# Kernel tuning notes

Hardware: AMD Instinct MI355X
Metric: run time of the kernel (lower is better)

The kernel has to match this reference:

```python
import jax, jax.numpy as jnp
import numpy as np

N = 100000   # nodes
E = 1600000  # edges (avg degree 16)
D = 128      # in = hidden = out channels
N_MID = 4    # middle GCN layers (layer_num=6 -> 1 in + 4 mid + 1 out)
BN_EPS = 1e-5


def setup_inputs() -> dict:
    key = jax.random.key(0)
    ks = jax.random.split(key, 6)
    scale = 1.0 / np.sqrt(D)
    x = jax.random.normal(ks[0], (N, D), dtype=jnp.float32)
    edge_index = jax.random.randint(ks[1], (2, E), 0, N, dtype=jnp.int64)
    W0 = jax.random.normal(ks[2], (D, D), dtype=jnp.float32) * scale
    Wmid = jax.random.normal(ks[3], (N_MID, D, D), dtype=jnp.float32) * scale
    Wlast = jax.random.normal(ks[4], (D, D), dtype=jnp.float32) * scale
    return {
        "x": x,
        "edge_index": edge_index,
        "W0": W0,
        "b0": jnp.zeros((D,), jnp.float32),
        "Wmid": Wmid,
        "bmid": jnp.zeros((N_MID, D), jnp.float32),
        "Wlast": Wlast,
        "blast": jnp.zeros((D,), jnp.float32),
        "gamma": jnp.ones((N_MID + 1, D), jnp.float32),
        "beta": jnp.zeros((N_MID + 1, D), jnp.float32),
    }


def _gcn_layer(x, W, b, src, dst, norm, n):
    # GCNConv: h = x @ W; out[dst] += norm_e * h[src]; + bias
    h = x @ W                         # [N, D_out]
    msg = h[src] * norm[:, None]      # [E+N, D_out] gathered + scaled
    return jax.ops.segment_sum(msg, dst, num_segments=n) + b


def _batchnorm(h, g, b):
    # training-mode BatchNorm1d over nodes (biased variance)
    mu = h.mean(axis=0)
    var = h.var(axis=0)
    return (h - mu) * jax.lax.rsqrt(var + BN_EPS) * g + b


def reference(x, edge_index, W0, b0, Wmid, bmid, Wlast, blast, gamma, beta):
    n = x.shape[0]
    # add self-loops (PyG GCNConv default), symmetric normalization
    loop = jnp.arange(n, dtype=edge_index.dtype)
    src = jnp.concatenate([edge_index[0], loop])
    dst = jnp.concatenate([edge_index[1], loop])
    deg = jax.ops.segment_sum(jnp.ones_like(src, dtype=x.dtype), dst, num_segments=n)
    dinv = jnp.where(deg > 0, deg ** -0.5, 0.0)
    norm = dinv[src] * dinv[dst]      # [E+N]

    # layer 0: no residual; dropout is identity in eval (deterministic reference)
    h = _gcn_layer(x, W0, b0, src, dst, norm, n)
    x = jax.nn.relu(_batchnorm(h, gamma[0], beta[0]))
    # middle layers: residual
    for i in range(N_MID):
        h = _gcn_layer(x, Wmid[i], bmid[i], src, dst, norm, n)
        x = jax.nn.relu(_batchnorm(h, gamma[i + 1], beta[i + 1])) + x
    # output layer: no norm/relu
    return _gcn_layer(x, Wlast, blast, src, dst, norm, n)
```

## Files before the change

### kernel.cpp

```cpp
#include <hip/hip_runtime.h>

#define D 128
#define BN_EPS 1e-5f

typedef _Float16 half8 __attribute__((ext_vector_type(8)));
typedef float f32x4 __attribute__((ext_vector_type(4)));
typedef unsigned short ushort_t;
typedef unsigned long long ull_t;

__device__ __forceinline__ unsigned short f2h(float f) {
  union { _Float16 h; unsigned short u; } c;
  c.h = (_Float16)f;
  return c.u;
}
__device__ __forceinline__ unsigned int packh(float lo, float hi) {
  return (unsigned int)f2h(lo) | ((unsigned int)f2h(hi) << 16);
}
__device__ __forceinline__ float h2f(unsigned int v) {
  union { unsigned short u; _Float16 h; } c;
  c.u = (unsigned short)v;
  return (float)c.h;
}

__global__ void k_detect(const int* __restrict__ ei, int* __restrict__ flag) {
  if (blockIdx.x == 0 && threadIdx.x == 0) {
    int is64 = 1;
    for (int i = 0; i < 16; i++)
      if (ei[2 * i + 1] != 0) is64 = 0;
    *flag = is64;
  }
}
__device__ __forceinline__ int load_src(const int* ei, int e, int i, int is64) {
  return is64 ? ei[2 * i] : ei[i];
}
__device__ __forceinline__ int load_dst(const int* ei, int e, int i, int is64) {
  return is64 ? ei[2 * e + 2 * i] : ei[e + i];
}

__global__ void k_hist(const int* __restrict__ ei, int* __restrict__ cnt,
                       const int* __restrict__ flag, int e) {
  int i = blockIdx.x * blockDim.x + threadIdx.x;
  if (i < e) {
    int d = load_dst(ei, e, i, *flag);
    atomicAdd(&cnt[d], 1);
  }
}

__global__ void k_dinv(const int* __restrict__ cnt, float* __restrict__ dinv, int n) {
  int i = blockIdx.x * blockDim.x + threadIdx.x;
  if (i < n) dinv[i] = rsqrtf((float)(cnt[i] + 1));
}

__global__ void k_ordA(const int* __restrict__ cnt, int* __restrict__ dfill,
                       int* __restrict__ bbase, int n, int nb) {
  __shared__ int h[256];
  int t = threadIdx.x;
  h[t] = 0;
  __syncthreads();
  int i = blockIdx.x * 256 + t;
  if (i < n) {
    int d = cnt[i];
    if (d > 255) d = 255;
    atomicAdd(&h[d], 1);
  }
  __syncthreads();
  int c = h[t];
  if (c) bbase[t * nb + blockIdx.x] = atomicAdd(&dfill[t], c);
}

__global__ void k_degscan(const int* __restrict__ dfill, int* __restrict__ dbase) {
  if (blockIdx.x == 0 && threadIdx.x == 0) {
    int run = 0;
    for (int i = 0; i < 256; i++) {
      int t = dfill[i];
      dbase[i] = run;
      run += t;
    }
  }
}

__global__ void k_ordB(const int* __restrict__ cnt, const int* __restrict__ dbase,
                       const int* __restrict__ bbase, unsigned int* __restrict__ ord,
                       int* __restrict__ rank, int* __restrict__ sdeg, int n,
                       int nb) {
  __shared__ int h[256];
  int t = threadIdx.x;
  h[t] = 0;
  __syncthreads();
  int i = blockIdx.x * 256 + t;
  if (i < n) {
    int dc = cnt[i];
    int d = dc > 255 ? 255 : dc;
    int loc = atomicAdd(&h[d], 1);
    int pos = dbase[d] + bbase[d * nb + blockIdx.x] + loc;
    ord[pos] = (unsigned int)i;
    rank[i] = pos;
    sdeg[pos] = dc + 1;
  }
}

__global__ void k_gscan(const int* __restrict__ sdeg, int* __restrict__ gbase,
                        int ngroups, int n) {
  __shared__ int s[256];
  int t = threadIdx.x;
  int per = (ngroups + 255) / 256;
  int g0 = t * per, g1 = g0 + per;
  if (g1 > ngroups) g1 = ngroups;
  int sum = 0;
  for (int g = g0; g < g1; g++) {
    int m = 0;
    for (int j = 0; j < 16; j++) {
      int idx = g * 16 + j;
      int v = (idx < n) ? sdeg[idx] : 0;
      m = max(m, v);
    }
    int st = (m + 1) & ~1;
    gbase[g] = st;
    sum += st * 16;
  }
  s[t] = sum;
  __syncthreads();
  for (int off = 1; off < 256; off <<= 1) {
    int x = (t >= off) ? s[t - off] : 0;
    __syncthreads();
    s[t] += x;
    __syncthreads();
  }
  int run = s[t] - sum;
  for (int g = g0; g < g1; g++) {
    int st = gbase[g];
    gbase[g] = run;
    run += st * 16;
  }
  if (t == 255) gbase[ngroups] = run;
}

__global__ void k_scatter(const int* __restrict__ ei, const int* __restrict__ rank,
                          const int* __restrict__ gbase, int* __restrict__ fill,
                          const float* __restrict__ dinv,
                          unsigned int* __restrict__ eh,
                          const int* __restrict__ flag, int e) {
  int i = blockIdx.x * blockDim.x + threadIdx.x;
  if (i < e) {
    int is64 = *flag;
    int s = load_src(ei, e, i, is64);
    int d = load_dst(ei, e, i, is64);
    int slot = atomicAdd(&fill[d], 1);
    int r = rank[d];
    int g = r >> 4, j = r & 15;
    unsigned int m = ((unsigned int)rank[s] << 15) |
                     (unsigned int)(f2h(dinv[s] * dinv[d]) & 0x7fff);
    __builtin_nontemporal_store(m, &eh[gbase[g] + slot * 16 + j]);
  }
}

__global__ void k_self(const int* __restrict__ cnt, const int* __restrict__ rank,
                       const int* __restrict__ gbase, const float* __restrict__ dinv,
                       unsigned int* __restrict__ eh, int n, int ntot) {
  int i = blockIdx.x * blockDim.x + threadIdx.x;
  if (i >= ntot) return;
  if (i < n) {
    float di = dinv[i];
    int r = rank[i];
    int g = r >> 4, j = r & 15;
    int gb = gbase[g];
    int stride = (gbase[g + 1] - gb) >> 4;
    unsigned int m = ((unsigned int)r << 15) |
                     (unsigned int)(f2h(di * di) & 0x7fff);
    int c = cnt[i];
    __builtin_nontemporal_store(m, &eh[gb + c * 16 + j]);
    for (int s = c + 1; s < stride; s++)
      __builtin_nontemporal_store(0u, &eh[gb + s * 16 + j]);
  } else {
    int g = i >> 4, j = i & 15;
    int gb = gbase[g];
    int stride = (gbase[g + 1] - gb) >> 4;
    for (int s = 0; s < stride; s++)
      __builtin_nontemporal_store(0u, &eh[gb + s * 16 + j]);
  }
}

__global__ void k_wconv(const float* __restrict__ W0, const float* __restrict__ Wmid,
                        const float* __restrict__ Wlast, ushort_t* __restrict__ Wf) {
  int i = blockIdx.x * 256 + threadIdx.x;
  if (i >= 6 * 16384) return;
  int l = i >> 14, r = i & 16383;
  int k = r >> 7, c = r & 127;
  const float* W = (l == 0) ? W0 : (l <= 4 ? Wmid + (size_t)(l - 1) * 16384 : Wlast);
  Wf[(size_t)l * 16384 + (((k >> 3) * 128 + c) << 3) + (k & 7)] = f2h(W[r]);
}

__global__ __launch_bounds__(256) void k_gemm(
    const void* __restrict__ src, const ushort_t* __restrict__ Wf,
    ushort_t* __restrict__ Hh, unsigned int* __restrict__ XhNew,
    const unsigned int* __restrict__ XhPrev, const float* __restrict__ stats,
    const float* __restrict__ gamma, const float* __restrict__ beta,
    const unsigned int* __restrict__ ord, int n, int mode) {
  __shared__ ushort_t As[16384];
  __shared__ ushort_t Ws[16384];
  const int t = threadIdx.x;
  const int rowBase = blockIdx.x * 128;
  const int off = t & 15;
  const size_t slice_stride = (size_t)n * 32;

  float sc[8], sh[8];
  if (mode >= 1) {
    float inv_n = 1.0f / (float)n;
#pragma unroll
    for (int j = 0; j < 8; j++) {
      int ch = off * 8 + j;
      float mean = stats[ch] * inv_n;
      float var = stats[128 + ch] * inv_n - mean * mean;
      if (var < 0.f) var = 0.f;
      float is = rsqrtf(var + BN_EPS);
      float s = gamma[ch] * is;
      sc[j] = s;
      sh[j] = beta[ch] - mean * s;
    }
  }

#pragma unroll
  for (int i = 0; i < 8; i++) {
    int c = t + i * 256;
    int row = c >> 4;
    int grow = rowBase + row;
    bool valid = grow < n;
    if (!valid) grow = n - 1;
    unsigned int pk[4];
    if (mode == 0) {
      int orig = (int)ord[grow];
      const float* xp = (const float*)src + (size_t)orig * 128 + off * 8;
      float4 v0 = *(const float4*)xp;
      float4 v1 = *(const float4*)(xp + 4);
      pk[0] = packh(v0.x, v0.y);
      pk[1] = packh(v0.z, v0.w);
      pk[2] = packh(v1.x, v1.y);
      pk[3] = packh(v1.z, v1.w);
    } else {
      const char* ap = (const char*)src + (size_t)(off >> 1) * slice_stride +
                       (size_t)grow * 32 + (off & 1) * 16;
      uint4 av = *(const uint4*)ap;
      float v[8];
      v[0] = h2f(av.x & 0xffff); v[1] = h2f(av.x >> 16);
      v[2] = h2f(av.y & 0xffff); v[3] = h2f(av.y >> 16);
      v[4] = h2f(av.z & 0xffff); v[5] = h2f(av.z >> 16);
      v[6] = h2f(av.w & 0xffff); v[7] = h2f(av.w >> 16);
#pragma unroll
      for (int j = 0; j < 8; j++) v[j] = fmaxf(v[j] * sc[j] + sh[j], 0.f);
      if (mode == 2) {
        uint4 rv = *(const uint4*)(XhPrev + (size_t)grow * 64 + off * 4);
        v[0] += h2f(rv.x & 0xffff); v[1] += h2f(rv.x >> 16);
        v[2] += h2f(rv.y & 0xffff); v[3] += h2f(rv.y >> 16);
        v[4] += h2f(rv.z & 0xffff); v[5] += h2f(rv.z >> 16);
        v[6] += h2f(rv.w & 0xffff); v[7] += h2f(rv.w >> 16);
      }
      pk[0] = packh(v[0], v[1]);
      pk[1] = packh(v[2], v[3]);
      pk[2] = packh(v[4], v[5]);
      pk[3] = packh(v[6], v[7]);
      if (valid) *(uint4*)(XhNew + (size_t)grow * 64 + off * 4) = *(uint4*)pk;
    }
    *(uint4*)(&As[(off * 128 + row) * 8]) = *(uint4*)pk;
  }
#pragma unroll
  for (int i = 0; i < 8; i++) {
    int c = t + i * 256;
    *(uint4*)(&Ws[c * 8]) = *(const uint4*)(Wf + c * 8);
  }
  __syncthreads();

  const int wave = t >> 6, lane = t & 63;
  const int q = lane >> 4, ln = lane & 15;
  const int m0 = wave * 32;

  f32x4 acc[2][8];
#pragma unroll
  for (int mt = 0; mt < 2; mt++)
#pragma unroll
    for (int nt = 0; nt < 8; nt++) acc[mt][nt] = (f32x4){0.f, 0.f, 0.f, 0.f};

#pragma unroll
  for (int kk = 0; kk < 4; kk++) {
    int kg = kk * 4 + q;
    half8 a[2];
#pragma unroll
    for (int mt = 0; mt < 2; mt++)
      a[mt] = *(const half8*)(&As[(kg * 128 + m0 + mt * 16 + ln) * 8]);
    half8 b[8];
#pragma unroll
    for (int nt = 0; nt < 8; nt++)
      b[nt] = *(const half8*)(&Ws[(kg * 128 + nt * 16 + ln) * 8]);
#pragma unroll
    for (int mt = 0; mt < 2; mt++)
#pragma unroll
      for (int nt = 0; nt < 8; nt++)
        acc[mt][nt] =
            __builtin_amdgcn_mfma_f32_16x16x32_f16(a[mt], b[nt], acc[mt][nt], 0, 0, 0);
  }

#pragma unroll
  for (int mt = 0; mt < 2; mt++) {
#pragma unroll
    for (int r = 0; r < 4; r++) {
      int grow = rowBase + m0 + mt * 16 + q * 4 + r;
      if (grow < n) {
#pragma unroll
        for (int nt = 0; nt < 8; nt++) {
          ushort_t* hp = (ushort_t*)((char*)Hh + (size_t)nt * slice_stride +
                                     (size_t)grow * 32);
          hp[ln] = f2h(acc[mt][nt][r]);
        }
      }
    }
  }
}

__global__ __launch_bounds__(256) void k_agg(const char* __restrict__ hb,
                                             const int* __restrict__ gbase,
                                             const unsigned int* __restrict__ eh,
                                             const unsigned int* __restrict__ ord,
                                             const float* __restrict__ bias,
                                             void* __restrict__ out,
                                             float* __restrict__ stats, int n,
                                             int ngroups, int last) {
  __shared__ float lsum[16], lsq[16];
  const int t = threadIdx.x;
  const int slice = blockIdx.x & 7;
  if (!last) {
    if (t < 16) {
      lsum[t] = 0.f;
      lsq[t] = 0.f;
    }
    __syncthreads();
  }
  const int wave = t >> 6, lane = t & 63;
  const int j = lane >> 2;
  const int c = lane & 3;
  const unsigned int c8 = (unsigned int)c * 8u;
  const size_t plane = (size_t)slice * (size_t)n * 32;
  const char* hbs = hb + plane;
  float4 bv = *(const float4*)(bias + slice * 16 + c * 4);
  float rs0 = 0.f, rs1 = 0.f, rs2 = 0.f, rs3 = 0.f;
  float rq0 = 0.f, rq1 = 0.f, rq2 = 0.f, rq3 = 0.f;

  union HU { uint2 u; _Float16 h[4]; };

  const int nstreams = (gridDim.x >> 3) * 4;
  const int sid = (blockIdx.x >> 3) * 4 + wave;

  for (int gi = sid; gi < ngroups; gi += nstreams) {
    int gb = gbase[gi];
    int dm = (gbase[gi + 1] - gb) >> 4;
    const unsigned int* mp = eh + gb + j;
    float a0 = 0.f, a1 = 0.f, a2 = 0.f, a3 = 0.f;
    int i = 0;
    for (; i + 4 <= dm; i += 4) {
      unsigned int m0 = mp[(i + 0) * 16];
      unsigned int m1 = mp[(i + 1) * 16];
      unsigned int m2 = mp[(i + 2) * 16];
      unsigned int m3 = mp[(i + 3) * 16];
      HU g0, g1, g2, g3;
      g0.u = *(const uint2*)(hbs + (((m0 >> 10) & ~31u) + c8));
      g1.u = *(const uint2*)(hbs + (((m1 >> 10) & ~31u) + c8));
      g2.u = *(const uint2*)(hbs + (((m2 >> 10) & ~31u) + c8));
      g3.u = *(const uint2*)(hbs + (((m3 >> 10) & ~31u) + c8));
      float w0 = h2f(m0 & 0x7fffu);
      float w1 = h2f(m1 & 0x7fffu);
      float w2 = h2f(m2 & 0x7fffu);
      float w3 = h2f(m3 & 0x7fffu);
      a0 = fmaf((float)g0.h[0], w0, a0);
      a1 = fmaf((float)g0.h[1], w0, a1);
      a2 = fmaf((float)g0.h[2], w0, a2);
      a3 = fmaf((float)g0.h[3], w0, a3);
      a0 = fmaf((float)g1.h[0], w1, a0);
      a1 = fmaf((float)g1.h[1], w1, a1);
      a2 = fmaf((float)g1.h[2], w1, a2);
      a3 = fmaf((float)g1.h[3], w1, a3);
      a0 = fmaf((float)g2.h[0], w2, a0);
      a1 = fmaf((float)g2.h[1], w2, a1);
      a2 = fmaf((float)g2.h[2], w2, a2);
      a3 = fmaf((float)g2.h[3], w2, a3);
      a0 = fmaf((float)g3.h[0], w3, a0);
      a1 = fmaf((float)g3.h[1], w3, a1);
      a2 = fmaf((float)g3.h[2], w3, a2);
      a3 = fmaf((float)g3.h[3], w3, a3);
    }
    if (i < dm) {
      unsigned int m0 = mp[(i + 0) * 16];
      unsigned int m1 = mp[(i + 1) * 16];
      HU g0, g1;
      g0.u = *(const uint2*)(hbs + (((m0 >> 10) & ~31u) + c8));
      g1.u = *(const uint2*)(hbs + (((m1 >> 10) & ~31u) + c8));
      float w0 = h2f(m0 & 0x7fffu);
      float w1 = h2f(m1 & 0x7fffu);
      a0 = fmaf((float)g0.h[0], w0, a0);
      a1 = fmaf((float)g0.h[1], w0, a1);
      a2 = fmaf((float)g0.h[2], w0, a2);
      a3 = fmaf((float)g0.h[3], w0, a3);
      a0 = fmaf((float)g1.h[0], w1, a0);
      a1 = fmaf((float)g1.h[1], w1, a1);
      a2 = fmaf((float)g1.h[2], w1, a2);
      a3 = fmaf((float)g1.h[3], w1, a3);
    }
    int oi = gi * 16 + j;
    if (oi < n) {
      a0 += bv.x;
      a1 += bv.y;
      a2 += bv.z;
      a3 += bv.w;
      if (last) {
        int nd = (int)ord[oi];
        float4 ov = {a0, a1, a2, a3};
        *(float4*)((float*)out + (size_t)nd * 128 + slice * 16 + c * 4) = ov;
      } else {
        uint2 ov;
        ov.x = packh(a0, a1);
        ov.y = packh(a2, a3);
        char* op = (char*)out + plane + (size_t)oi * 32 + c8;
        __builtin_nontemporal_store(((unsigned long long)ov.y << 32) | ov.x,
                                    (unsigned long long*)op);
        rs0 += a0; rs1 += a1; rs2 += a2; rs3 += a3;
        rq0 += a0 * a0; rq1 += a1 * a1; rq2 += a2 * a2; rq3 += a3 * a3;
      }
    }
  }

  if (!last) {
    rs0 += __shfl_xor(rs0, 4);  rs1 += __shfl_xor(rs1, 4);
    rs2 += __shfl_xor(rs2, 4);  rs3 += __shfl_xor(rs3, 4);
    rq0 += __shfl_xor(rq0, 4);  rq1 += __shfl_xor(rq1, 4);
    rq2 += __shfl_xor(rq2, 4);  rq3 += __shfl_xor(rq3, 4);
    rs0 += __shfl_xor(rs0, 8);  rs1 += __shfl_xor(rs1, 8);
    rs2 += __shfl_xor(rs2, 8);  rs3 += __shfl_xor(rs3, 8);
    rq0 += __shfl_xor(rq0, 8);  rq1 += __shfl_xor(rq1, 8);
    rq2 += __shfl_xor(rq2, 8);  rq3 += __shfl_xor(rq3, 8);
    rs0 += __shfl_xor(rs0, 16); rs1 += __shfl_xor(rs1, 16);
    rs2 += __shfl_xor(rs2, 16); rs3 += __shfl_xor(rs3, 16);
    rq0 += __shfl_xor(rq0, 16); rq1 += __shfl_xor(rq1, 16);
    rq2 += __shfl_xor(rq2, 16); rq3 += __shfl_xor(rq3, 16);
    rs0 += __shfl_xor(rs0, 32); rs1 += __shfl_xor(rs1, 32);
    rs2 += __shfl_xor(rs2, 32); rs3 += __shfl_xor(rs3, 32);
    rq0 += __shfl_xor(rq0, 32); rq1 += __shfl_xor(rq1, 32);
    rq2 += __shfl_xor(rq2, 32); rq3 += __shfl_xor(rq3, 32);
    if (lane < 4) {
      atomicAdd(&lsum[c * 4 + 0], rs0);
      atomicAdd(&lsum[c * 4 + 1], rs1);
      atomicAdd(&lsum[c * 4 + 2], rs2);
      atomicAdd(&lsum[c * 4 + 3], rs3);
      atomicAdd(&lsq[c * 4 + 0], rq0);
      atomicAdd(&lsq[c * 4 + 1], rq1);
      atomicAdd(&lsq[c * 4 + 2], rq2);
      atomicAdd(&lsq[c * 4 + 3], rq3);
    }
    __syncthreads();
    if (t < 16) {
      atomicAdd(&stats[slice * 16 + t], lsum[t]);
      atomicAdd(&stats[128 + slice * 16 + t], lsq[t]);
    }
  }
}

extern "C" void kernel_launch(void* const* d_in, const int* in_sizes, int n_in,
                              void* d_out, int out_size, void* d_ws, size_t ws_size,
                              hipStream_t stream) {
  const float* x_in = (const float*)d_in[0];
  const int* ei = (const int*)d_in[1];
  const float* W0 = (const float*)d_in[2];
  const float* b0 = (const float*)d_in[3];
  const float* Wmid = (const float*)d_in[4];
  const float* bmid = (const float*)d_in[5];
  const float* Wlast = (const float*)d_in[6];
  const float* blast = (const float*)d_in[7];
  const float* gamma = (const float*)d_in[8];
  const float* beta = (const float*)d_in[9];

  const int n = in_sizes[0] / D;
  const int e = in_sizes[1] / 2;
  const int ngroups = (n + 15) / 16;
  const int ntot = ngroups * 16;
  const int nb = (n + 255) / 256;
  const int ec = e + 10 * n;

  char* ws = (char*)d_ws;
  size_t off = 0;
  auto alloc = [&](size_t bytes) -> void* {
    void* p = ws + off;
    off += (bytes + 255) & ~(size_t)255;
    return p;
  };
  unsigned int* XhA = (unsigned int*)alloc((size_t)n * 64 * 4);
  unsigned int* XhB = (unsigned int*)alloc((size_t)n * 64 * 4);
  unsigned int* Hh = (unsigned int*)alloc((size_t)n * 64 * 4);
  unsigned int* Ag = (unsigned int*)alloc((size_t)n * 64 * 4);
  ushort_t* Wf = (ushort_t*)alloc((size_t)6 * 16384 * 2);
  float* dinv = (float*)alloc((size_t)n * 4);
  int* flag = (int*)alloc(256);
  unsigned int* ord = (unsigned int*)alloc((size_t)ntot * 4);
  int* rank = (int*)alloc((size_t)n * 4);
  int* gbase = (int*)alloc((size_t)(ngroups + 1) * 4);
  int* dbase = (int*)alloc(256 * 4);
  int* bbase = (int*)alloc((size_t)256 * nb * 4);
  unsigned int* eh = (unsigned int*)alloc((size_t)ec * 4);
  int* sdeg = (int*)alloc((size_t)ntot * 4);
  char* zbase = ws + off;
  int* cnt = (int*)alloc((size_t)n * 4);
  int* fill = (int*)alloc((size_t)n * 4);
  int* dfill = (int*)alloc(256 * 4);
  float* stats = (float*)alloc(5 * 256 * 4);
  size_t zbytes = (size_t)((ws + off) - zbase);
  hipMemsetAsync(zbase, 0, zbytes, stream);

  k_detect<<<1, 64, 0, stream>>>(ei, flag);
  int eb = (e + 255) / 256;
  k_hist<<<eb, 256, 0, stream>>>(ei, cnt, flag, e);
  k_dinv<<<nb, 256, 0, stream>>>(cnt, dinv, n);
  k_ordA<<<nb, 256, 0, stream>>>(cnt, dfill, bbase, n, nb);
  k_degscan<<<1, 64, 0, stream>>>(dfill, dbase);
  k_ordB<<<nb, 256, 0, stream>>>(cnt, dbase, bbase, ord, rank, sdeg, n, nb);
  k_gscan<<<1, 256, 0, stream>>>(sdeg, gbase, ngroups, n);
  k_scatter<<<eb, 256, 0, stream>>>(ei, rank, gbase, fill, dinv, eh, flag, e);
  k_self<<<(ntot + 255) / 256, 256, 0, stream>>>(cnt, rank, gbase, dinv, eh, n,
                                                 ntot);
  k_wconv<<<(6 * 16384 + 255) / 256, 256, 0, stream>>>(W0, Wmid, Wlast, Wf);

  const int gemm_blocks = (n + 127) / 128;
  const int agg_blocks = 2048;

  k_gemm<<<gemm_blocks, 256, 0, stream>>>(x_in, Wf, (ushort_t*)Hh, nullptr,
                                          nullptr, nullptr, nullptr, nullptr,
                                          ord, n, 0);
  k_agg<<<agg_blocks, 256, 0, stream>>>((const char*)Hh, gbase, eh, ord, b0, Ag,
                                        stats, n, ngroups, 0);
  unsigned int* xprev = nullptr;
  unsigned int* xnew = XhA;
  for (int L = 1; L <= 4; L++) {
    const float* bL = bmid + (size_t)(L - 1) * D;
    k_gemm<<<gemm_blocks, 256, 0, stream>>>(
        Ag, Wf + (size_t)L * 16384, (ushort_t*)Hh, xnew, xprev,
        stats + (L - 1) * 256, gamma + (L - 1) * D, beta + (L - 1) * D, ord, n,
        (L == 1) ? 1 : 2);
    k_agg<<<agg_blocks, 256, 0, stream>>>((const char*)Hh, gbase, eh, ord, bL,
                                          Ag, stats + L * 256, n, ngroups, 0);
    xprev = xnew;
    xnew = (xnew == XhA) ? XhB : XhA;
  }
  k_gemm<<<gemm_blocks, 256, 0, stream>>>(Ag, Wf + (size_t)5 * 16384,
                                          (ushort_t*)Hh, xnew, xprev,
                                          stats + 4 * 256, gamma + 4 * D,
                                          beta + 4 * D, ord, n, 2);
  k_agg<<<agg_blocks, 256, 0, stream>>>((const char*)Hh, gbase, eh, ord, blast,
                                        d_out, nullptr, n, ngroups, 1);
}
```

Before: 958.3 us.

## Zero edge buffer via memset, plain stores, and unroll aggregation by eight

The padded edge-slot buffer now sits inside the memset-zeroed workspace region, so k_self no longer loops writing zeros into padding slots and only writes the self-loop entry. Scatter and self-loop writes switch from nontemporal to ordinary stores. The aggregation inner loop is unrolled to eight edges per iteration, with a four-step and a two-step tail, so more gathers are in flight. In exchange the memset grows by the full edge buffer size, and the wider unroll raises register pressure in k_agg.

```diff
diff --git a/kernel.cpp b/kernel.cpp
--- a/kernel.cpp
+++ b/kernel.cpp
@@ -150,33 +150,21 @@
     int g = r >> 4, j = r & 15;
     unsigned int m = ((unsigned int)rank[s] << 15) |
                      (unsigned int)(f2h(dinv[s] * dinv[d]) & 0x7fff);
-    __builtin_nontemporal_store(m, &eh[gbase[g] + slot * 16 + j]);
+    eh[gbase[g] + slot * 16 + j] = m;
   }
 }
 
 __global__ void k_self(const int* __restrict__ cnt, const int* __restrict__ rank,
                        const int* __restrict__ gbase, const float* __restrict__ dinv,
-                       unsigned int* __restrict__ eh, int n, int ntot) {
+                       unsigned int* __restrict__ eh, int n) {
   int i = blockIdx.x * blockDim.x + threadIdx.x;
-  if (i >= ntot) return;
   if (i < n) {
     float di = dinv[i];
     int r = rank[i];
     int g = r >> 4, j = r & 15;
-    int gb = gbase[g];
-    int stride = (gbase[g + 1] - gb) >> 4;
     unsigned int m = ((unsigned int)r << 15) |
                      (unsigned int)(f2h(di * di) & 0x7fff);
-    int c = cnt[i];
-    __builtin_nontemporal_store(m, &eh[gb + c * 16 + j]);
-    for (int s = c + 1; s < stride; s++)
-      __builtin_nontemporal_store(0u, &eh[gb + s * 16 + j]);
-  } else {
-    int g = i >> 4, j = i & 15;
-    int gb = gbase[g];
-    int stride = (gbase[g + 1] - gb) >> 4;
-    for (int s = 0; s < stride; s++)
-      __builtin_nontemporal_store(0u, &eh[gb + s * 16 + j]);
+    eh[gbase[g] + cnt[i] * 16 + j] = m;
   }
 }
 
@@ -315,6 +303,18 @@
   }
 }
 
+#define STEP(K)                                                   \
+  {                                                               \
+    unsigned int m_ = mp[(i + K) * 16];                           \
+    HU g_;                                                        \
+    g_.u = *(const uint2*)(hbs + (((m_ >> 10) & ~31u) + c8));     \
+    float w_ = h2f(m_ & 0x7fffu);                                 \
+    a0 = fmaf((float)g_.h[0], w_, a0);                            \
+    a1 = fmaf((float)g_.h[1], w_, a1);                            \
+    a2 = fmaf((float)g_.h[2], w_, a2);                            \
+    a3 = fmaf((float)g_.h[3], w_, a3);                            \
+  }
+
 __global__ __launch_bounds__(256) void k_agg(const char* __restrict__ hb,
                                              const int* __restrict__ gbase,
                                              const unsigned int* __restrict__ eh,
@@ -354,53 +354,51 @@
     const unsigned int* mp = eh + gb + j;
     float a0 = 0.f, a1 = 0.f, a2 = 0.f, a3 = 0.f;
     int i = 0;
-    for (; i + 4 <= dm; i += 4) {
+    for (; i + 8 <= dm; i += 8) {
       unsigned int m0 = mp[(i + 0) * 16];
       unsigned int m1 = mp[(i + 1) * 16];
       unsigned int m2 = mp[(i + 2) * 16];
       unsigned int m3 = mp[(i + 3) * 16];
-      HU g0, g1, g2, g3;
+      unsigned int m4 = mp[(i + 4) * 16];
+      unsigned int m5 = mp[(i + 5) * 16];
+      unsigned int m6 = mp[(i + 6) * 16];
+      unsigned int m7 = mp[(i + 7) * 16];
+      HU g0, g1, g2, g3, g4, g5, g6, g7;
       g0.u = *(const uint2*)(hbs + (((m0 >> 10) & ~31u) + c8));
       g1.u = *(const uint2*)(hbs + (((m1 >> 10) & ~31u) + c8));
       g2.u = *(const uint2*)(hbs + (((m2 >> 10) & ~31u) + c8));
       g3.u = *(const uint2*)(hbs + (((m3 >> 10) & ~31u) + c8));
-      float w0 = h2f(m0 & 0x7fffu);
-      float w1 = h2f(m1 & 0x7fffu);
-      float w2 = h2f(m2 & 0x7fffu);
-      float w3 = h2f(m3 & 0x7fffu);
-      a0 = fmaf((float)g0.h[0], w0, a0);
-      a1 = fmaf((float)g0.h[1], w0, a1);
-      a2 = fmaf((float)g0.h[2], w0, a2);
-      a3 = fmaf((float)g0.h[3], w0, a3);
-      a0 = fmaf((float)g1.h[0], w1, a0);
-      a1 = fmaf((float)g1.h[1], w1, a1);
-      a2 = fmaf((float)g1.h[2], w1, a2);
-      a3 = fmaf((float)g1.h[3], w1, a3);
-      a0 = fmaf((float)g2.h[0], w2, a0);
-      a1 = fmaf((float)g2.h[1], w2, a1);
-      a2 = fmaf((float)g2.h[2], w2, a2);
-      a3 = fmaf((float)g2.h[3], w2, a3);
-      a0 = fmaf((float)g3.h[0], w3, a0);
-      a1 = fmaf((float)g3.h[1], w3, a1);
-      a2 = fmaf((float)g3.h[2], w3, a2);
-      a3 = fmaf((float)g3.h[3], w3, a3);
+      g4.u = *(const uint2*)(hbs + (((m4 >> 10) & ~31u) + c8));
+      g5.u = *(const uint2*)(hbs + (((m5 >> 10) & ~31u) + c8));
+      g6.u = *(const uint2*)(hbs + (((m6 >> 10) & ~31u) + c8));
+      g7.u = *(const uint2*)(hbs + (((m7 >> 10) & ~31u) + c8));
+      float w0 = h2f(m0 & 0x7fffu), w1 = h2f(m1 & 0x7fffu);
+      float w2 = h2f(m2 & 0x7fffu), w3 = h2f(m3 & 0x7fffu);
+      float w4 = h2f(m4 & 0x7fffu), w5 = h2f(m5 & 0x7fffu);
+      float w6 = h2f(m6 & 0x7fffu), w7 = h2f(m7 & 0x7fffu);
+      a0 = fmaf((float)g0.h[0], w0, a0); a1 = fmaf((float)g0.h[1], w0, a1);
+      a2 = fmaf((float)g0.h[2], w0, a2); a3 = fmaf((float)g0.h[3], w0, a3);
+      a0 = fmaf((float)g1.h[0], w1, a0); a1 = fmaf((float)g1.h[1], w1, a1);
+      a2 = fmaf((float)g1.h[2], w1, a2); a3 = fmaf((float)g1.h[3], w1, a3);
+      a0 = fmaf((float)g2.h[0], w2, a0); a1 = fmaf((float)g2.h[1], w2, a1);
+      a2 = fmaf((float)g2.h[2], w2, a2); a3 = fmaf((float)g2.h[3], w2, a3);
+      a0 = fmaf((float)g3.h[0], w3, a0); a1 = fmaf((float)g3.h[1], w3, a1);
+      a2 = fmaf((float)g3.h[2], w3, a2); a3 = fmaf((float)g3.h[3], w3, a3);
+      a0 = fmaf((float)g4.h[0], w4, a0); a1 = fmaf((float)g4.h[1], w4, a1);
+      a2 = fmaf((float)g4.h[2], w4, a2); a3 = fmaf((float)g4.h[3], w4, a3);
+      a0 = fmaf((float)g5.h[0], w5, a0); a1 = fmaf((float)g5.h[1], w5, a1);
+      a2 = fmaf((float)g5.h[2], w5, a2); a3 = fmaf((float)g5.h[3], w5, a3);
+      a0 = fmaf((float)g6.h[0], w6, a0); a1 = fmaf((float)g6.h[1], w6, a1);
+      a2 = fmaf((float)g6.h[2], w6, a2); a3 = fmaf((float)g6.h[3], w6, a3);
+      a0 = fmaf((float)g7.h[0], w7, a0); a1 = fmaf((float)g7.h[1], w7, a1);
+      a2 = fmaf((float)g7.h[2], w7, a2); a3 = fmaf((float)g7.h[3], w7, a3);
+    }
+    if (i + 4 <= dm) {
+      STEP(0) STEP(1) STEP(2) STEP(3)
+      i += 4;
     }
     if (i < dm) {
-      unsigned int m0 = mp[(i + 0) * 16];
-      unsigned int m1 = mp[(i + 1) * 16];
-      HU g0, g1;
-      g0.u = *(const uint2*)(hbs + (((m0 >> 10) & ~31u) + c8));
-      g1.u = *(const uint2*)(hbs + (((m1 >> 10) & ~31u) + c8));
-      float w0 = h2f(m0 & 0x7fffu);
-      float w1 = h2f(m1 & 0x7fffu);
-      a0 = fmaf((float)g0.h[0], w0, a0);
-      a1 = fmaf((float)g0.h[1], w0, a1);
-      a2 = fmaf((float)g0.h[2], w0, a2);
-      a3 = fmaf((float)g0.h[3], w0, a3);
-      a0 = fmaf((float)g1.h[0], w1, a0);
-      a1 = fmaf((float)g1.h[1], w1, a1);
-      a2 = fmaf((float)g1.h[2], w1, a2);
-      a3 = fmaf((float)g1.h[3], w1, a3);
+      STEP(0) STEP(1)
     }
     int oi = gi * 16 + j;
     if (oi < n) {
@@ -459,6 +457,7 @@
     }
   }
 }
+#undef STEP
 
 extern "C" void kernel_launch(void* const* d_in, const int* in_sizes, int n_in,
                               void* d_out, int out_size, void* d_ws, size_t ws_size,
@@ -500,9 +499,9 @@
   int* gbase = (int*)alloc((size_t)(ngroups + 1) * 4);
   int* dbase = (int*)alloc(256 * 4);
   int* bbase = (int*)alloc((size_t)256 * nb * 4);
-  unsigned int* eh = (unsigned int*)alloc((size_t)ec * 4);
   int* sdeg = (int*)alloc((size_t)ntot * 4);
   char* zbase = ws + off;
+  unsigned int* eh = (unsigned int*)alloc((size_t)ec * 4);
   int* cnt = (int*)alloc((size_t)n * 4);
   int* fill = (int*)alloc((size_t)n * 4);
   int* dfill = (int*)alloc(256 * 4);
@@ -519,8 +518,7 @@
   k_ordB<<<nb, 256, 0, stream>>>(cnt, dbase, bbase, ord, rank, sdeg, n, nb);
   k_gscan<<<1, 256, 0, stream>>>(sdeg, gbase, ngroups, n);
   k_scatter<<<eb, 256, 0, stream>>>(ei, rank, gbase, fill, dinv, eh, flag, e);
-  k_self<<<(ntot + 255) / 256, 256, 0, stream>>>(cnt, rank, gbase, dinv, eh, n,
-                                                 ntot);
+  k_self<<<nb, 256, 0, stream>>>(cnt, rank, gbase, dinv, eh, n);
   k_wconv<<<(6 * 16384 + 255) / 256, 256, 0, stream>>>(W0, Wmid, Wlast, Wf);
 
   const int gemm_blocks = (n + 127) / 128;
```

After: 934.8 us. -2.5%, faster.
